# Optimization experiments

Hardware: AMD Instinct MI355X
Metric: run time of the kernel (lower is better)

The kernel has to match this reference:

```python
import jax, jax.numpy as jnp
import numpy as np

N_NODES = 50000
N_EDGES = 800000
D_IN = 128
D_HID = 128
N_LAYERS = 3
BN_EPS = 1e-5


def setup_inputs() -> dict:
    key = jax.random.key(0)
    ks = jax.random.split(key, 12)
    x = jax.random.normal(ks[0], (N_NODES, D_IN), dtype=jnp.float32)
    edge_index = jax.random.randint(ks[1], (2, N_EDGES), 0, N_NODES, dtype=jnp.int64)
    edge_weight = jax.random.uniform(ks[2], (N_EDGES,), dtype=jnp.float32)
    s1 = 1.0 / np.sqrt(D_IN)
    s2 = 1.0 / np.sqrt(D_HID)
    # stacked per-layer GIN MLP params (layer 0 in_dim == hidden_dim so stacking is valid)
    W1s = jax.random.uniform(ks[3], (N_LAYERS, D_HID, D_HID), jnp.float32, -s1, s1)
    b1s = jax.random.uniform(ks[4], (N_LAYERS, D_HID), jnp.float32, -s1, s1)
    W2s = jax.random.uniform(ks[5], (N_LAYERS, D_HID, D_HID), jnp.float32, -s2, s2)
    b2s = jax.random.uniform(ks[6], (N_LAYERS, D_HID), jnp.float32, -s2, s2)
    eps = jnp.zeros((N_LAYERS,), jnp.float32)  # GINConv eps init 0
    gamma = jnp.ones((D_HID,), jnp.float32)
    beta = jnp.zeros((D_HID,), jnp.float32)
    Wp = jax.random.uniform(ks[7], (D_HID, D_HID), jnp.float32, -s2, s2)
    bp = jax.random.uniform(ks[8], (D_HID,), jnp.float32, -s2, s2)
    prelu_a = jnp.asarray(0.25, jnp.float32)
    return {"x": x, "edge_weight": edge_weight, "W1s": W1s, "b1s": b1s,
            "W2s": W2s, "b2s": b2s, "eps": eps, "gamma": gamma, "beta": beta,
            "Wp": Wp, "bp": bp, "prelu_a": prelu_a, "edge_index": edge_index}


def reference(x, edge_weight, W1s, b1s, W2s, b2s, eps, gamma, beta, Wp, bp, prelu_a, edge_index):
    src, dst = edge_index[0], edge_index[1]
    z = x
    for i in range(N_LAYERS):
        # GINConv: sum-aggregate weighted neighbor messages, then 2-layer MLP
        msg = z[src] * edge_weight[:, None]                       # [E, d]
        agg = jax.ops.segment_sum(msg, dst, num_segments=N_NODES)  # [N, d]
        h = (1.0 + eps[i]) * z + agg
        h = jax.nn.relu(h @ W1s[i] + b1s[i]) @ W2s[i] + b2s[i]
        z = jax.nn.relu(h)  # activation; dropout inactive (eval)
    # BatchNorm1d (training-mode batch statistics, biased variance)
    mean = jnp.mean(z, axis=0)
    var = jnp.var(z, axis=0)
    zn = (z - mean) * jax.lax.rsqrt(var + BN_EPS) * gamma + beta
    # projection head: Linear -> PReLU (dropout inactive)
    p = zn @ Wp + bp
    p = jnp.where(p >= 0, p, prelu_a * p)
    return zn, p
```

## Files before the change

kernel.cpp:

```cpp
#include <hip/hip_runtime.h>
#include <hip/hip_fp16.h>

#define N_NODES 50000
#define N_EDGES 800000
#define D 128
#define ND (N_NODES * D)
#define BN_EPS 1e-5f

#define NB 256
#define NPB 196
#define BCAP 4096

typedef short bf16x8 __attribute__((ext_vector_type(8)));
typedef _Float16 f16x8 __attribute__((ext_vector_type(8)));
typedef float f32x4 __attribute__((ext_vector_type(4)));
typedef unsigned short u16x8 __attribute__((ext_vector_type(8)));

__device__ inline unsigned short f2bf(float f) {
    unsigned int u = __float_as_uint(f);
    u += 0x7FFF + ((u >> 16) & 1);
    return (unsigned short)(u >> 16);
}
__device__ inline float bf2f(unsigned short h) {
    return __uint_as_float(((unsigned int)h) << 16);
}
__device__ inline unsigned short f2h(float f) {
    return __half_as_ushort(__float2half(f));
}
__device__ inline float h2f(unsigned short u) {
    return __half2float(__ushort_as_half(u));
}
__device__ inline f16x8 as_f16x8(u16x8 v) {
    union { u16x8 u; f16x8 f; } x; x.u = v; return x.f;
}

__global__ void convert_x(const float* __restrict__ x, ushort* __restrict__ xh) {
    int i = (blockIdx.x * blockDim.x + threadIdx.x) * 4;
    if (i < ND) {
        float4 v = *(const float4*)(x + i);
        *(ushort4*)(xh + i) = make_ushort4(f2h(v.x), f2h(v.y), f2h(v.z), f2h(v.w));
    }
}

__global__ void pack_w_split(const float* __restrict__ W1s, const float* __restrict__ W2s,
                             const float* __restrict__ Wp, ushort* __restrict__ out) {
    int idx = blockIdx.x * blockDim.x + threadIdx.x;
    if (idx >= 7 * 16384) return;
    int m = idx >> 14;
    int p = idx & 16383;
    int c = p >> 11;
    int kc = (p >> 9) & 3;
    int lane = (p >> 3) & 63;
    int j = p & 7;
    int k = kc * 32 + (lane >> 4) * 8 + j;
    int col = c * 16 + (lane & 15);
    const float* src = (m < 3) ? (W1s + (size_t)m * 16384)
                     : (m < 6) ? (W2s + (size_t)(m - 3) * 16384)
                               : Wp;
    float v = src[k * 128 + col];
    if (m < 3) {
        unsigned short hi = f2h(v);
        float r = (v - h2f(hi)) * 2048.0f;
        out[(size_t)(2 * m) * 16384 + p] = hi;
        out[(size_t)(2 * m + 1) * 16384 + p] = f2h(r);
    } else {
        unsigned short hi = f2bf(v);
        float r = v - bf2f(hi);
        out[(size_t)(2 * m) * 16384 + p] = hi;
        out[(size_t)(2 * m + 1) * 16384 + p] = f2bf(r);
    }
}

__global__ void hist_kernel(const int* __restrict__ dst, int* __restrict__ offs) {
    int e = blockIdx.x * blockDim.x + threadIdx.x;
    if (e < N_EDGES) atomicAdd(&offs[dst[e] + 1], 1);
}

__global__ void scan_kernel(int* __restrict__ offs, int* __restrict__ bcur) {
    __shared__ int wsum[16];
    __shared__ int carry_s;
    int tid = threadIdx.x;
    int lane = tid & 63;
    int wave = tid >> 6;
    if (tid == 0) carry_s = 0;
    __syncthreads();
    for (int base = 1; base <= N_NODES; base += 8192) {
        int i0 = base + tid * 8;
        int v[8];
        #pragma unroll
        for (int k = 0; k < 8; ++k) {
            int idx = i0 + k;
            v[k] = (idx <= N_NODES) ? offs[idx] : 0;
        }
        #pragma unroll
        for (int k = 1; k < 8; ++k) v[k] += v[k - 1];
        int tsum = v[7];
        int x = tsum;
        #pragma unroll
        for (int d = 1; d < 64; d <<= 1) {
            int y = __shfl_up(x, d, 64);
            if (lane >= d) x += y;
        }
        if (lane == 63) wsum[wave] = x;
        __syncthreads();
        if (wave == 0 && lane < 16) {
            int y = wsum[lane];
            #pragma unroll
            for (int d = 1; d < 16; d <<= 1) {
                int t = __shfl_up(y, d, 64);
                if (lane >= d) y += t;
            }
            wsum[lane] = y;
        }
        __syncthreads();
        int waveoff = (wave > 0) ? wsum[wave - 1] : 0;
        int total = wsum[15];
        int add = (x - tsum) + waveoff + carry_s;
        #pragma unroll
        for (int k = 0; k < 8; ++k) {
            int idx = i0 + k;
            if (idx <= N_NODES) offs[idx] = v[k] + add;
        }
        __syncthreads();
        if (tid == 0) carry_s += total;
        __syncthreads();
    }
    if (tid < NB) bcur[tid] = offs[tid * NPB];
}

__global__ __launch_bounds__(256) void bucket_scatter(
    const int* __restrict__ src, const int* __restrict__ dst,
    const float* __restrict__ ew, int* __restrict__ bcur,
    uint2* __restrict__ pay) {
    __shared__ int cnt[NB];
    __shared__ int cur[NB];
    int tid = threadIdx.x;
    for (int i = tid; i < NB; i += 256) cnt[i] = 0;
    __syncthreads();
    int base = blockIdx.x * 2048;
    int s[8], d[8], b[8];
    float w[8];
    #pragma unroll
    for (int k = 0; k < 8; ++k) {
        int e = base + k * 256 + tid;
        bool v = e < N_EDGES;
        d[k] = v ? dst[e] : 0;
        s[k] = v ? src[e] : 0;
        w[k] = v ? ew[e] : 0.f;
        b[k] = d[k] / NPB;
        if (v) atomicAdd(&cnt[b[k]], 1);
    }
    __syncthreads();
    for (int i = tid; i < NB; i += 256) {
        int c = cnt[i];
        cur[i] = (c > 0) ? atomicAdd(&bcur[i], c) : 0;
    }
    __syncthreads();
    #pragma unroll
    for (int k = 0; k < 8; ++k) {
        int e = base + k * 256 + tid;
        if (e < N_EDGES) {
            int bk = b[k];
            int p = atomicAdd(&cur[bk], 1);
            unsigned dloc = (unsigned)(d[k] - bk * NPB);
            pay[p] = make_uint2((unsigned)s[k] | (dloc << 17), __float_as_uint(w[k]));
        }
    }
}

__global__ __launch_bounds__(256) void bucket_sort(const int* __restrict__ offs,
                                                   uint2* __restrict__ pay) {
    __shared__ uint2 lp[BCAP];
    __shared__ int cur[NPB];
    int b = blockIdx.x;
    int tid = threadIdx.x;
    int n0 = b * NPB;
    int n1 = min(n0 + NPB, N_NODES);
    int nn = n1 - n0;
    int r0 = offs[n0];
    int r1 = offs[n1];
    for (int i = tid; i < nn; i += 256) cur[i] = offs[n0 + i] - r0;
    __syncthreads();
    int cnt = r1 - r0;
    for (int i = tid; i < cnt; i += 256) {
        uint2 e = pay[r0 + i];
        int dloc = (int)(e.x >> 17);
        int p = atomicAdd(&cur[dloc], 1);
        if (p < BCAP) lp[p] = make_uint2(e.x & 0x1FFFFu, e.y);
    }
    __syncthreads();
    for (int i = tid; i < cnt; i += 256) {
        if (i < BCAP) pay[r0 + i] = lp[i];
    }
}

__global__ void gather_agg_f16(const ushort* __restrict__ z, const int* __restrict__ offs,
                               const uint2* __restrict__ pay,
                               const float* __restrict__ epsp, int layer,
                               ushort* __restrict__ A) {
    int tid = blockIdx.x * blockDim.x + threadIdx.x;
    int n = tid >> 5;
    if (n >= N_NODES) return;
    int f = (tid & 31) << 2;
    float epsv = 1.0f + epsp[layer];
    int beg = offs[n], end = offs[n + 1];
    ushort4 zi = *(const ushort4*)(z + (size_t)n * D + f);
    float ax = epsv * h2f(zi.x), ay = epsv * h2f(zi.y);
    float az = epsv * h2f(zi.z), aw = epsv * h2f(zi.w);
    int j = beg;
    for (; j + 4 <= end; j += 4) {
        uint2 e0 = pay[j];
        uint2 e1 = pay[j + 1];
        uint2 e2 = pay[j + 2];
        uint2 e3 = pay[j + 3];
        ushort4 v0 = *(const ushort4*)(z + (size_t)e0.x * D + f);
        ushort4 v1 = *(const ushort4*)(z + (size_t)e1.x * D + f);
        ushort4 v2 = *(const ushort4*)(z + (size_t)e2.x * D + f);
        ushort4 v3 = *(const ushort4*)(z + (size_t)e3.x * D + f);
        float w0 = __uint_as_float(e0.y);
        float w1 = __uint_as_float(e1.y);
        float w2 = __uint_as_float(e2.y);
        float w3 = __uint_as_float(e3.y);
        ax += h2f(v0.x) * w0 + h2f(v1.x) * w1 + h2f(v2.x) * w2 + h2f(v3.x) * w3;
        ay += h2f(v0.y) * w0 + h2f(v1.y) * w1 + h2f(v2.y) * w2 + h2f(v3.y) * w3;
        az += h2f(v0.z) * w0 + h2f(v1.z) * w1 + h2f(v2.z) * w2 + h2f(v3.z) * w3;
        aw += h2f(v0.w) * w0 + h2f(v1.w) * w1 + h2f(v2.w) * w2 + h2f(v3.w) * w3;
    }
    for (; j < end; ++j) {
        uint2 e0 = pay[j];
        ushort4 v0 = *(const ushort4*)(z + (size_t)e0.x * D + f);
        float w0 = __uint_as_float(e0.y);
        ax += h2f(v0.x) * w0; ay += h2f(v0.y) * w0;
        az += h2f(v0.z) * w0; aw += h2f(v0.w) * w0;
    }
    *(ushort4*)(A + (size_t)n * D + f) = make_ushort4(f2h(ax), f2h(ay), f2h(az), f2h(aw));
}

#define HSTR 132
template<bool STATS>
__global__ __launch_bounds__(256) void mlp_fused(
    const ushort* __restrict__ A,
    const ushort* __restrict__ W1hi, const ushort* __restrict__ W1lo,
    const float* __restrict__ b1,
    const ushort* __restrict__ W2hi, const ushort* __restrict__ W2lo,
    const float* __restrict__ b2, ushort* __restrict__ Z,
    float* __restrict__ stats) {
    __shared__ float Hs[4][16 * HSTR];
    __shared__ float red[256];
    int tid = threadIdx.x;
    int lane = tid & 63;
    int wave = tid >> 6;
    int rlo = lane & 15;
    int quad = lane >> 4;
    int blk0 = blockIdx.x * 64;
    int row0 = blk0 + wave * 16;
    int arow = row0 + rlo;
    int ar = (arow < N_NODES) ? arow : (N_NODES - 1);

    const f16x8* W1h = (const f16x8*)W1hi;
    const f16x8* W1l = (const f16x8*)W1lo;
    const bf16x8* W2h = (const bf16x8*)W2hi;
    const bf16x8* W2l = (const bf16x8*)W2lo;

    f16x8 af[4];
    #pragma unroll
    for (int kc = 0; kc < 4; ++kc) {
        u16x8 raw = *(const u16x8*)(A + (size_t)ar * D + kc * 32 + quad * 8);
        af[kc] = as_f16x8(raw);
    }

    f32x4 acc[8];
    #pragma unroll
    for (int c = 0; c < 8; ++c) {
        f32x4 aH = (f32x4){0.f, 0.f, 0.f, 0.f};
        f32x4 aL = (f32x4){0.f, 0.f, 0.f, 0.f};
        #pragma unroll
        for (int kc = 0; kc < 4; ++kc) {
            f16x8 wh = W1h[(c * 4 + kc) * 64 + lane];
            f16x8 wl = W1l[(c * 4 + kc) * 64 + lane];
            aH = __builtin_amdgcn_mfma_f32_16x16x32_f16(af[kc], wh, aH, 0, 0, 0);
            aL = __builtin_amdgcn_mfma_f32_16x16x32_f16(af[kc], wl, aL, 0, 0, 0);
        }
        acc[c] = aH + aL * (1.0f / 2048.0f);
    }

    #pragma unroll
    for (int c = 0; c < 8; ++c) {
        int col = c * 16 + rlo;
        float bb = b1[col];
        #pragma unroll
        for (int r = 0; r < 4; ++r) {
            Hs[wave][(quad * 4 + r) * HSTR + col] = fmaxf(acc[c][r] + bb, 0.f);
        }
    }
    __syncthreads();

    bf16x8 a2hi[4], a2lo[4];
    #pragma unroll
    for (int kc = 0; kc < 4; ++kc) {
        const float* p = &Hs[wave][rlo * HSTR + kc * 32 + quad * 8];
        #pragma unroll
        for (int j = 0; j < 8; ++j) {
            float v = p[j];
            unsigned short h = f2bf(v);
            a2hi[kc][j] = (short)h;
            a2lo[kc][j] = (short)f2bf(v - bf2f(h));
        }
    }

    f32x4 acc2[8];
    #pragma unroll
    for (int c = 0; c < 8; ++c) acc2[c] = (f32x4){0.f, 0.f, 0.f, 0.f};
    #pragma unroll
    for (int c = 0; c < 8; ++c) {
        #pragma unroll
        for (int kc = 0; kc < 4; ++kc) {
            bf16x8 wh = W2h[(c * 4 + kc) * 64 + lane];
            bf16x8 wl = W2l[(c * 4 + kc) * 64 + lane];
            acc2[c] = __builtin_amdgcn_mfma_f32_16x16x32_bf16(a2lo[kc], wh, acc2[c], 0, 0, 0);
            acc2[c] = __builtin_amdgcn_mfma_f32_16x16x32_bf16(a2hi[kc], wl, acc2[c], 0, 0, 0);
            acc2[c] = __builtin_amdgcn_mfma_f32_16x16x32_bf16(a2hi[kc], wh, acc2[c], 0, 0, 0);
        }
    }

    __syncthreads();
    #pragma unroll
    for (int c = 0; c < 8; ++c) {
        int col = c * 16 + rlo;
        float bb = b2[col];
        #pragma unroll
        for (int r = 0; r < 4; ++r) {
            Hs[wave][(quad * 4 + r) * HSTR + col] = fmaxf(acc2[c][r] + bb, 0.f);
        }
    }
    __syncthreads();
    #pragma unroll
    for (int p2 = 0; p2 < 4; ++p2) {
        int r = p2 * 4 + quad;
        int grow = row0 + r;
        if (grow < N_NODES) {
            float4 lo = *(const float4*)&Hs[wave][r * HSTR + rlo * 8];
            float4 hi = *(const float4*)&Hs[wave][r * HSTR + rlo * 8 + 4];
            ushort us[8] = {f2h(lo.x), f2h(lo.y), f2h(lo.z), f2h(lo.w),
                            f2h(hi.x), f2h(hi.y), f2h(hi.z), f2h(hi.w)};
            *(float4*)(Z + (size_t)grow * D + rlo * 8) = *(const float4*)us;
        }
    }

    if (STATS) {
        int col = tid & 127;
        int half = tid >> 7;
        float s = 0.f, s2 = 0.f;
        #pragma unroll
        for (int i = 0; i < 32; ++i) {
            int row = half * 32 + i;
            if (blk0 + row < N_NODES) {
                float v = Hs[row >> 4][(row & 15) * HSTR + col];
                s += v;
                s2 += v * v;
            }
        }
        red[tid] = s;
        __syncthreads();
        if (half == 0) atomicAdd(&stats[col], s + red[tid + 128]);
        __syncthreads();
        red[tid] = s2;
        __syncthreads();
        if (half == 0) atomicAdd(&stats[D + col], s2 + red[tid + 128]);
    }
}

#define PSTR 132
__global__ __launch_bounds__(256) void bn_proj(
    const ushort* __restrict__ Z, const float* __restrict__ stats,
    const float* __restrict__ gamma, const float* __restrict__ beta,
    const ushort* __restrict__ Wphi, const ushort* __restrict__ Wplo,
    const float* __restrict__ bp, const float* __restrict__ prelu_a,
    float* __restrict__ zn_out, float* __restrict__ p_out) {
    __shared__ float sc_s[D];
    __shared__ float sh_s[D];
    __shared__ float Ps[4][16 * PSTR];
    int tid = threadIdx.x;
    int lane = tid & 63;
    int wave = tid >> 6;
    int rlo = lane & 15;
    int quad = lane >> 4;

    if (tid < D) {
        float m = stats[tid] * (1.0f / N_NODES);
        float v = stats[D + tid] * (1.0f / N_NODES) - m * m;
        float rs = rsqrtf(v + BN_EPS);
        float sc = rs * gamma[tid];
        sc_s[tid] = sc;
        sh_s[tid] = beta[tid] - m * sc;
    }
    __syncthreads();

    int row0 = blockIdx.x * 64 + wave * 16;
    int arow = row0 + rlo;
    int ar = (arow < N_NODES) ? arow : (N_NODES - 1);

    const bf16x8* Wh = (const bf16x8*)Wphi;
    const bf16x8* Wl = (const bf16x8*)Wplo;

    bf16x8 ahi[4], alo[4];
    #pragma unroll
    for (int kc = 0; kc < 4; ++kc) {
        u16x8 raw = *(const u16x8*)(Z + (size_t)ar * D + kc * 32 + quad * 8);
        float zn[8];
        #pragma unroll
        for (int j = 0; j < 8; ++j) {
            int k = kc * 32 + quad * 8 + j;
            zn[j] = sc_s[k] * h2f(raw[j]) + sh_s[k];
            unsigned short h = f2bf(zn[j]);
            ahi[kc][j] = (short)h;
            alo[kc][j] = (short)f2bf(zn[j] - bf2f(h));
        }
        if (arow < N_NODES) {
            float* dst = zn_out + (size_t)arow * D + kc * 32 + quad * 8;
            *(float4*)dst = make_float4(zn[0], zn[1], zn[2], zn[3]);
            *(float4*)(dst + 4) = make_float4(zn[4], zn[5], zn[6], zn[7]);
        }
    }

    f32x4 acc[8];
    #pragma unroll
    for (int c = 0; c < 8; ++c) acc[c] = (f32x4){0.f, 0.f, 0.f, 0.f};
    #pragma unroll
    for (int c = 0; c < 8; ++c) {
        #pragma unroll
        for (int kc = 0; kc < 4; ++kc) {
            bf16x8 wh = Wh[(c * 4 + kc) * 64 + lane];
            bf16x8 wl = Wl[(c * 4 + kc) * 64 + lane];
            acc[c] = __builtin_amdgcn_mfma_f32_16x16x32_bf16(alo[kc], wh, acc[c], 0, 0, 0);
            acc[c] = __builtin_amdgcn_mfma_f32_16x16x32_bf16(ahi[kc], wl, acc[c], 0, 0, 0);
            acc[c] = __builtin_amdgcn_mfma_f32_16x16x32_bf16(ahi[kc], wh, acc[c], 0, 0, 0);
        }
    }

    float aP = prelu_a[0];
    #pragma unroll
    for (int c = 0; c < 8; ++c) {
        int col = c * 16 + rlo;
        float bb = bp[col];
        #pragma unroll
        for (int r = 0; r < 4; ++r) {
            float v = acc[c][r] + bb;
            v = (v >= 0.f) ? v : aP * v;
            Ps[wave][(quad * 4 + r) * PSTR + col] = v;
        }
    }
    __syncthreads();
    #pragma unroll
    for (int p2 = 0; p2 < 8; ++p2) {
        int r = p2 * 2 + (lane >> 5);
        int grow = row0 + r;
        if (grow < N_NODES) {
            *(float4*)(p_out + (size_t)grow * D + (lane & 31) * 4) =
                *(const float4*)&Ps[wave][r * PSTR + (lane & 31) * 4];
        }
    }
}

extern "C" void kernel_launch(void* const* d_in, const int* in_sizes, int n_in,
                              void* d_out, int out_size, void* d_ws, size_t ws_size,
                              hipStream_t stream) {
    (void)in_sizes; (void)n_in; (void)out_size; (void)ws_size;
    const float* x     = (const float*)d_in[0];
    const float* ew    = (const float*)d_in[1];
    const float* W1s   = (const float*)d_in[2];
    const float* b1s   = (const float*)d_in[3];
    const float* W2s   = (const float*)d_in[4];
    const float* b2s   = (const float*)d_in[5];
    const float* eps   = (const float*)d_in[6];
    const float* gamma = (const float*)d_in[7];
    const float* beta  = (const float*)d_in[8];
    const float* Wp    = (const float*)d_in[9];
    const float* bp    = (const float*)d_in[10];
    const float* pa    = (const float*)d_in[11];
    const int*   ei    = (const int*)d_in[12];
    const int* srcp = ei;
    const int* dstp = ei + N_EDGES;

    char* wsb = (char*)d_ws;
    float*  stats  = (float*)wsb;                 wsb += 1024;
    int*    offs   = (int*)wsb;                   wsb += 200016;
    int*    bcur   = (int*)wsb;                   wsb += 200016;
    uint2*  pay    = (uint2*)wsb;                 wsb += 6400000;
    ushort* Wpk    = (ushort*)wsb;                wsb += 14 * 16384 * 2;
    ushort* Xh     = (ushort*)wsb;                wsb += (size_t)ND * 2;
    ushort* Ah     = (ushort*)wsb;                wsb += (size_t)ND * 2;
    ushort* Zh     = (ushort*)wsb;                wsb += (size_t)ND * 2;

    float* out_zn = (float*)d_out;
    float* out_p  = out_zn + ND;

    hipMemsetAsync(stats, 0, 256 * sizeof(float), stream);
    hipMemsetAsync(offs, 0, (N_NODES + 1) * sizeof(int), stream);

    convert_x<<<(ND / 4 + 255) / 256, 256, 0, stream>>>(x, Xh);
    pack_w_split<<<(7 * 16384 + 255) / 256, 256, 0, stream>>>(W1s, W2s, Wp, Wpk);

    hist_kernel<<<(N_EDGES + 255) / 256, 256, 0, stream>>>(dstp, offs);
    scan_kernel<<<1, 1024, 0, stream>>>(offs, bcur);
    bucket_scatter<<<(N_EDGES + 2047) / 2048, 256, 0, stream>>>(srcp, dstp, ew, bcur, pay);
    bucket_sort<<<NB, 256, 0, stream>>>(offs, pay);

    int mgrid = (N_NODES + 63) / 64;
    const ushort* zin = Xh;
    for (int l = 0; l < 3; ++l) {
        gather_agg_f16<<<(N_NODES * 32 + 255) / 256, 256, 0, stream>>>(zin, offs, pay, eps, l, Ah);
        if (l < 2) {
            mlp_fused<false><<<mgrid, 256, 0, stream>>>(Ah,
                Wpk + (size_t)(2 * l) * 16384,       Wpk + (size_t)(2 * l + 1) * 16384, b1s + (size_t)l * D,
                Wpk + (size_t)(2 * (3 + l)) * 16384, Wpk + (size_t)(2 * (3 + l) + 1) * 16384, b2s + (size_t)l * D,
                Zh, stats);
        } else {
            mlp_fused<true><<<mgrid, 256, 0, stream>>>(Ah,
                Wpk + (size_t)(2 * l) * 16384,       Wpk + (size_t)(2 * l + 1) * 16384, b1s + (size_t)l * D,
                Wpk + (size_t)(2 * (3 + l)) * 16384, Wpk + (size_t)(2 * (3 + l) + 1) * 16384, b2s + (size_t)l * D,
                Zh, stats);
        }
        zin = Zh;
    }
    bn_proj<<<mgrid, 256, 0, stream>>>(Zh, stats, gamma, beta,
        Wpk + (size_t)12 * 16384, Wpk + (size_t)13 * 16384, bp, pa, out_zn, out_p);
}
```

Baseline: 413.2 us.

## Restructure GIN MLP kernel to one wave per block with two row tiles

The fused MLP kernel now uses 64-thread blocks, and each wave processes 32 rows as two 16-row MFMA fragments. Each weight fragment loaded from global memory is therefore reused across twice as many rows. The batch-norm statistics are now reduced with cross-lane shuffles inside the output loop instead of a shared-memory reduction over 256 threads, so the block-level barriers go away. In exchange, register pressure per wave goes up and the grid has twice as many small blocks, which shifts occupancy and the rate of atomic updates to the statistics buffer.

```diff
diff --git a/kernel.cpp b/kernel.cpp
--- a/kernel.cpp
+++ b/kernel.cpp
@@ -238,135 +238,134 @@
 
 #define HSTR 132
 template<bool STATS>
-__global__ __launch_bounds__(256) void mlp_fused(
+__global__ __launch_bounds__(64) void mlp_fused(
     const ushort* __restrict__ A,
     const ushort* __restrict__ W1hi, const ushort* __restrict__ W1lo,
     const float* __restrict__ b1,
     const ushort* __restrict__ W2hi, const ushort* __restrict__ W2lo,
     const float* __restrict__ b2, ushort* __restrict__ Z,
     float* __restrict__ stats) {
-    __shared__ float Hs[4][16 * HSTR];
-    __shared__ float red[256];
-    int tid = threadIdx.x;
-    int lane = tid & 63;
-    int wave = tid >> 6;
+    __shared__ float Hs[32 * HSTR];
+    int lane = threadIdx.x;
     int rlo = lane & 15;
     int quad = lane >> 4;
-    int blk0 = blockIdx.x * 64;
-    int row0 = blk0 + wave * 16;
-    int arow = row0 + rlo;
-    int ar = (arow < N_NODES) ? arow : (N_NODES - 1);
+    int row0 = blockIdx.x * 32;
 
     const f16x8* W1h = (const f16x8*)W1hi;
     const f16x8* W1l = (const f16x8*)W1lo;
     const bf16x8* W2h = (const bf16x8*)W2hi;
     const bf16x8* W2l = (const bf16x8*)W2lo;
 
-    f16x8 af[4];
-    #pragma unroll
-    for (int kc = 0; kc < 4; ++kc) {
-        u16x8 raw = *(const u16x8*)(A + (size_t)ar * D + kc * 32 + quad * 8);
-        af[kc] = as_f16x8(raw);
-    }
-
-    f32x4 acc[8];
+    f16x8 af[2][4];
+    #pragma unroll
+    for (int rf = 0; rf < 2; ++rf) {
+        int arow = row0 + rf * 16 + rlo;
+        int ar = (arow < N_NODES) ? arow : (N_NODES - 1);
+        #pragma unroll
+        for (int kc = 0; kc < 4; ++kc) {
+            u16x8 raw = *(const u16x8*)(A + (size_t)ar * D + kc * 32 + quad * 8);
+            af[rf][kc] = as_f16x8(raw);
+        }
+    }
+
     #pragma unroll
     for (int c = 0; c < 8; ++c) {
-        f32x4 aH = (f32x4){0.f, 0.f, 0.f, 0.f};
-        f32x4 aL = (f32x4){0.f, 0.f, 0.f, 0.f};
+        f32x4 aH0 = (f32x4){0.f, 0.f, 0.f, 0.f};
+        f32x4 aL0 = (f32x4){0.f, 0.f, 0.f, 0.f};
+        f32x4 aH1 = (f32x4){0.f, 0.f, 0.f, 0.f};
+        f32x4 aL1 = (f32x4){0.f, 0.f, 0.f, 0.f};
         #pragma unroll
         for (int kc = 0; kc < 4; ++kc) {
             f16x8 wh = W1h[(c * 4 + kc) * 64 + lane];
             f16x8 wl = W1l[(c * 4 + kc) * 64 + lane];
-            aH = __builtin_amdgcn_mfma_f32_16x16x32_f16(af[kc], wh, aH, 0, 0, 0);
-            aL = __builtin_amdgcn_mfma_f32_16x16x32_f16(af[kc], wl, aL, 0, 0, 0);
-        }
-        acc[c] = aH + aL * (1.0f / 2048.0f);
-    }
-
-    #pragma unroll
-    for (int c = 0; c < 8; ++c) {
+            aH0 = __builtin_amdgcn_mfma_f32_16x16x32_f16(af[0][kc], wh, aH0, 0, 0, 0);
+            aH1 = __builtin_amdgcn_mfma_f32_16x16x32_f16(af[1][kc], wh, aH1, 0, 0, 0);
+            aL0 = __builtin_amdgcn_mfma_f32_16x16x32_f16(af[0][kc], wl, aL0, 0, 0, 0);
+            aL1 = __builtin_amdgcn_mfma_f32_16x16x32_f16(af[1][kc], wl, aL1, 0, 0, 0);
+        }
         int col = c * 16 + rlo;
         float bb = b1[col];
         #pragma unroll
         for (int r = 0; r < 4; ++r) {
-            Hs[wave][(quad * 4 + r) * HSTR + col] = fmaxf(acc[c][r] + bb, 0.f);
-        }
-    }
-    __syncthreads();
-
-    bf16x8 a2hi[4], a2lo[4];
-    #pragma unroll
-    for (int kc = 0; kc < 4; ++kc) {
-        const float* p = &Hs[wave][rlo * HSTR + kc * 32 + quad * 8];
-        #pragma unroll
-        for (int j = 0; j < 8; ++j) {
-            float v = p[j];
-            unsigned short h = f2bf(v);
-            a2hi[kc][j] = (short)h;
-            a2lo[kc][j] = (short)f2bf(v - bf2f(h));
-        }
-    }
-
-    f32x4 acc2[8];
-    #pragma unroll
-    for (int c = 0; c < 8; ++c) acc2[c] = (f32x4){0.f, 0.f, 0.f, 0.f};
+            Hs[(quad * 4 + r) * HSTR + col]        = fmaxf(aH0[r] + aL0[r] * (1.0f / 2048.0f) + bb, 0.f);
+            Hs[(16 + quad * 4 + r) * HSTR + col]   = fmaxf(aH1[r] + aL1[r] * (1.0f / 2048.0f) + bb, 0.f);
+        }
+    }
+    __syncthreads();
+
+    bf16x8 a2hi[2][4], a2lo[2][4];
+    #pragma unroll
+    for (int rf = 0; rf < 2; ++rf) {
+        #pragma unroll
+        for (int kc = 0; kc < 4; ++kc) {
+            const float* p = &Hs[(rf * 16 + rlo) * HSTR + kc * 32 + quad * 8];
+            #pragma unroll
+            for (int j = 0; j < 8; ++j) {
+                float v = p[j];
+                unsigned short h = f2bf(v);
+                a2hi[rf][kc][j] = (short)h;
+                a2lo[rf][kc][j] = (short)f2bf(v - bf2f(h));
+            }
+        }
+    }
+    __syncthreads();
+
     #pragma unroll
     for (int c = 0; c < 8; ++c) {
+        f32x4 ac0 = (f32x4){0.f, 0.f, 0.f, 0.f};
+        f32x4 ac1 = (f32x4){0.f, 0.f, 0.f, 0.f};
         #pragma unroll
         for (int kc = 0; kc < 4; ++kc) {
             bf16x8 wh = W2h[(c * 4 + kc) * 64 + lane];
             bf16x8 wl = W2l[(c * 4 + kc) * 64 + lane];
-            acc2[c] = __builtin_amdgcn_mfma_f32_16x16x32_bf16(a2lo[kc], wh, acc2[c], 0, 0, 0);
-            acc2[c] = __builtin_amdgcn_mfma_f32_16x16x32_bf16(a2hi[kc], wl, acc2[c], 0, 0, 0);
-            acc2[c] = __builtin_amdgcn_mfma_f32_16x16x32_bf16(a2hi[kc], wh, acc2[c], 0, 0, 0);
-        }
-    }
-
-    __syncthreads();
-    #pragma unroll
-    for (int c = 0; c < 8; ++c) {
+            ac0 = __builtin_amdgcn_mfma_f32_16x16x32_bf16(a2lo[0][kc], wh, ac0, 0, 0, 0);
+            ac1 = __builtin_amdgcn_mfma_f32_16x16x32_bf16(a2lo[1][kc], wh, ac1, 0, 0, 0);
+            ac0 = __builtin_amdgcn_mfma_f32_16x16x32_bf16(a2hi[0][kc], wl, ac0, 0, 0, 0);
+            ac1 = __builtin_amdgcn_mfma_f32_16x16x32_bf16(a2hi[1][kc], wl, ac1, 0, 0, 0);
+            ac0 = __builtin_amdgcn_mfma_f32_16x16x32_bf16(a2hi[0][kc], wh, ac0, 0, 0, 0);
+            ac1 = __builtin_amdgcn_mfma_f32_16x16x32_bf16(a2hi[1][kc], wh, ac1, 0, 0, 0);
+        }
         int col = c * 16 + rlo;
         float bb = b2[col];
+        float s = 0.f, s2 = 0.f;
         #pragma unroll
         for (int r = 0; r < 4; ++r) {
-            Hs[wave][(quad * 4 + r) * HSTR + col] = fmaxf(acc2[c][r] + bb, 0.f);
-        }
-    }
-    __syncthreads();
-    #pragma unroll
-    for (int p2 = 0; p2 < 4; ++p2) {
-        int r = p2 * 4 + quad;
+            float v0 = fmaxf(ac0[r] + bb, 0.f);
+            float v1 = fmaxf(ac1[r] + bb, 0.f);
+            Hs[(quad * 4 + r) * HSTR + col] = v0;
+            Hs[(16 + quad * 4 + r) * HSTR + col] = v1;
+            if (STATS) {
+                float m0 = (row0 + quad * 4 + r < N_NODES) ? v0 : 0.f;
+                float m1 = (row0 + 16 + quad * 4 + r < N_NODES) ? v1 : 0.f;
+                s += m0 + m1;
+                s2 += m0 * m0 + m1 * m1;
+            }
+        }
+        if (STATS) {
+            s  += __shfl_xor(s, 16, 64);
+            s  += __shfl_xor(s, 32, 64);
+            s2 += __shfl_xor(s2, 16, 64);
+            s2 += __shfl_xor(s2, 32, 64);
+            if (lane < 16) {
+                atomicAdd(&stats[col], s);
+                atomicAdd(&stats[D + col], s2);
+            }
+        }
+    }
+    __syncthreads();
+
+    #pragma unroll
+    for (int it = 0; it < 8; ++it) {
+        int r = it * 4 + quad;
         int grow = row0 + r;
         if (grow < N_NODES) {
-            float4 lo = *(const float4*)&Hs[wave][r * HSTR + rlo * 8];
-            float4 hi = *(const float4*)&Hs[wave][r * HSTR + rlo * 8 + 4];
+            const float* p = &Hs[r * HSTR + rlo * 8];
+            float4 lo = *(const float4*)p;
+            float4 hi = *(const float4*)(p + 4);
             ushort us[8] = {f2h(lo.x), f2h(lo.y), f2h(lo.z), f2h(lo.w),
                             f2h(hi.x), f2h(hi.y), f2h(hi.z), f2h(hi.w)};
             *(float4*)(Z + (size_t)grow * D + rlo * 8) = *(const float4*)us;
         }
-    }
-
-    if (STATS) {
-        int col = tid & 127;
-        int half = tid >> 7;
-        float s = 0.f, s2 = 0.f;
-        #pragma unroll
-        for (int i = 0; i < 32; ++i) {
-            int row = half * 32 + i;
-            if (blk0 + row < N_NODES) {
-                float v = Hs[row >> 4][(row & 15) * HSTR + col];
-                s += v;
-                s2 += v * v;
-            }
-        }
-        red[tid] = s;
-        __syncthreads();
-        if (half == 0) atomicAdd(&stats[col], s + red[tid + 128]);
-        __syncthreads();
-        red[tid] = s2;
-        __syncthreads();
-        if (half == 0) atomicAdd(&stats[D + col], s2 + red[tid + 128]);
     }
 }
 
@@ -506,23 +505,24 @@
     bucket_scatter<<<(N_EDGES + 2047) / 2048, 256, 0, stream>>>(srcp, dstp, ew, bcur, pay);
     bucket_sort<<<NB, 256, 0, stream>>>(offs, pay);
 
-    int mgrid = (N_NODES + 63) / 64;
+    int mgrid = (N_NODES + 31) / 32;
+    int pgrid = (N_NODES + 63) / 64;
     const ushort* zin = Xh;
     for (int l = 0; l < 3; ++l) {
         gather_agg_f16<<<(N_NODES * 32 + 255) / 256, 256, 0, stream>>>(zin, offs, pay, eps, l, Ah);
         if (l < 2) {
-            mlp_fused<false><<<mgrid, 256, 0, stream>>>(Ah,
+            mlp_fused<false><<<mgrid, 64, 0, stream>>>(Ah,
                 Wpk + (size_t)(2 * l) * 16384,       Wpk + (size_t)(2 * l + 1) * 16384, b1s + (size_t)l * D,
                 Wpk + (size_t)(2 * (3 + l)) * 16384, Wpk + (size_t)(2 * (3 + l) + 1) * 16384, b2s + (size_t)l * D,
                 Zh, stats);
         } else {
-            mlp_fused<true><<<mgrid, 256, 0, stream>>>(Ah,
+            mlp_fused<true><<<mgrid, 64, 0, stream>>>(Ah,
                 Wpk + (size_t)(2 * l) * 16384,       Wpk + (size_t)(2 * l + 1) * 16384, b1s + (size_t)l * D,
                 Wpk + (size_t)(2 * (3 + l)) * 16384, Wpk + (size_t)(2 * (3 + l) + 1) * 16384, b2s + (size_t)l * D,
                 Zh, stats);
         }
         zin = Zh;
     }
-    bn_proj<<<mgrid, 256, 0, stream>>>(Zh, stats, gamma, beta,
+    bn_proj<<<pgrid, 256, 0, stream>>>(Zh, stats, gamma, beta,
         Wpk + (size_t)12 * 16384, Wpk + (size_t)13 * 16384, bp, pa, out_zn, out_p);
 }
```

Measured after the change: 437.0 us. 1.06x slower.

## Split MLP columns across waves so each weight fragment serves four row tiles

Applied to the files above, without the earlier changes.

Each wave in the fused GIN MLP kernel used to own 16 rows and loaded every weight fragment for all 128 output columns. Now each wave owns 32 output columns for all 64 rows of the block, so each weight fragment is loaded once and used in four MFMAs. The hidden activations are shared through one block-wide LDS tile, and the BatchNorm statistics are reduced inside the epilogue with cross-lane shuffles instead of a separate LDS reduction pass. In exchange, each wave now loads A fragments for all 64 rows and keeps more accumulators live, which raises register pressure.

```diff
diff --git a/kernel.cpp b/kernel.cpp
--- a/kernel.cpp
+++ b/kernel.cpp
@@ -245,128 +245,143 @@
     const ushort* __restrict__ W2hi, const ushort* __restrict__ W2lo,
     const float* __restrict__ b2, ushort* __restrict__ Z,
     float* __restrict__ stats) {
-    __shared__ float Hs[4][16 * HSTR];
-    __shared__ float red[256];
+    __shared__ float Hs[64 * HSTR];
     int tid = threadIdx.x;
     int lane = tid & 63;
     int wave = tid >> 6;
     int rlo = lane & 15;
     int quad = lane >> 4;
     int blk0 = blockIdx.x * 64;
-    int row0 = blk0 + wave * 16;
-    int arow = row0 + rlo;
-    int ar = (arow < N_NODES) ? arow : (N_NODES - 1);
 
     const f16x8* W1h = (const f16x8*)W1hi;
     const f16x8* W1l = (const f16x8*)W1lo;
     const bf16x8* W2h = (const bf16x8*)W2hi;
     const bf16x8* W2l = (const bf16x8*)W2lo;
 
-    f16x8 af[4];
-    #pragma unroll
-    for (int kc = 0; kc < 4; ++kc) {
-        u16x8 raw = *(const u16x8*)(A + (size_t)ar * D + kc * 32 + quad * 8);
-        af[kc] = as_f16x8(raw);
-    }
-
-    f32x4 acc[8];
-    #pragma unroll
-    for (int c = 0; c < 8; ++c) {
-        f32x4 aH = (f32x4){0.f, 0.f, 0.f, 0.f};
-        f32x4 aL = (f32x4){0.f, 0.f, 0.f, 0.f};
+    f16x8 af[4][4];
+    #pragma unroll
+    for (int rf = 0; rf < 4; ++rf) {
+        int arow = blk0 + rf * 16 + rlo;
+        int ar = (arow < N_NODES) ? arow : (N_NODES - 1);
+        #pragma unroll
+        for (int kc = 0; kc < 4; ++kc) {
+            u16x8 raw = *(const u16x8*)(A + (size_t)ar * D + kc * 32 + quad * 8);
+            af[rf][kc] = as_f16x8(raw);
+        }
+    }
+
+    #pragma unroll
+    for (int cc = 0; cc < 2; ++cc) {
+        int c = 2 * wave + cc;
+        f32x4 aH[4], aL[4];
+        #pragma unroll
+        for (int rf = 0; rf < 4; ++rf) {
+            aH[rf] = (f32x4){0.f, 0.f, 0.f, 0.f};
+            aL[rf] = (f32x4){0.f, 0.f, 0.f, 0.f};
+        }
         #pragma unroll
         for (int kc = 0; kc < 4; ++kc) {
             f16x8 wh = W1h[(c * 4 + kc) * 64 + lane];
             f16x8 wl = W1l[(c * 4 + kc) * 64 + lane];
-            aH = __builtin_amdgcn_mfma_f32_16x16x32_f16(af[kc], wh, aH, 0, 0, 0);
-            aL = __builtin_amdgcn_mfma_f32_16x16x32_f16(af[kc], wl, aL, 0, 0, 0);
-        }
-        acc[c] = aH + aL * (1.0f / 2048.0f);
-    }
-
-    #pragma unroll
-    for (int c = 0; c < 8; ++c) {
+            #pragma unroll
+            for (int rf = 0; rf < 4; ++rf) {
+                aH[rf] = __builtin_amdgcn_mfma_f32_16x16x32_f16(af[rf][kc], wh, aH[rf], 0, 0, 0);
+                aL[rf] = __builtin_amdgcn_mfma_f32_16x16x32_f16(af[rf][kc], wl, aL[rf], 0, 0, 0);
+            }
+        }
         int col = c * 16 + rlo;
         float bb = b1[col];
         #pragma unroll
-        for (int r = 0; r < 4; ++r) {
-            Hs[wave][(quad * 4 + r) * HSTR + col] = fmaxf(acc[c][r] + bb, 0.f);
-        }
-    }
-    __syncthreads();
-
-    bf16x8 a2hi[4], a2lo[4];
+        for (int rf = 0; rf < 4; ++rf) {
+            #pragma unroll
+            for (int r = 0; r < 4; ++r) {
+                Hs[(rf * 16 + quad * 4 + r) * HSTR + col] =
+                    fmaxf(aH[rf][r] + aL[rf][r] * (1.0f / 2048.0f) + bb, 0.f);
+            }
+        }
+    }
+    __syncthreads();
+
+    f32x4 acc2[2][4];
+    #pragma unroll
+    for (int cc = 0; cc < 2; ++cc)
+        #pragma unroll
+        for (int rf = 0; rf < 4; ++rf)
+            acc2[cc][rf] = (f32x4){0.f, 0.f, 0.f, 0.f};
+
     #pragma unroll
     for (int kc = 0; kc < 4; ++kc) {
-        const float* p = &Hs[wave][rlo * HSTR + kc * 32 + quad * 8];
-        #pragma unroll
-        for (int j = 0; j < 8; ++j) {
-            float v = p[j];
-            unsigned short h = f2bf(v);
-            a2hi[kc][j] = (short)h;
-            a2lo[kc][j] = (short)f2bf(v - bf2f(h));
-        }
-    }
-
-    f32x4 acc2[8];
-    #pragma unroll
-    for (int c = 0; c < 8; ++c) acc2[c] = (f32x4){0.f, 0.f, 0.f, 0.f};
-    #pragma unroll
-    for (int c = 0; c < 8; ++c) {
-        #pragma unroll
-        for (int kc = 0; kc < 4; ++kc) {
+        bf16x8 a2hi[4], a2lo[4];
+        #pragma unroll
+        for (int rf = 0; rf < 4; ++rf) {
+            const float* p = &Hs[(rf * 16 + rlo) * HSTR + kc * 32 + quad * 8];
+            #pragma unroll
+            for (int j = 0; j < 8; ++j) {
+                float v = p[j];
+                unsigned short h = f2bf(v);
+                a2hi[rf][j] = (short)h;
+                a2lo[rf][j] = (short)f2bf(v - bf2f(h));
+            }
+        }
+        #pragma unroll
+        for (int cc = 0; cc < 2; ++cc) {
+            int c = 2 * wave + cc;
             bf16x8 wh = W2h[(c * 4 + kc) * 64 + lane];
             bf16x8 wl = W2l[(c * 4 + kc) * 64 + lane];
-            acc2[c] = __builtin_amdgcn_mfma_f32_16x16x32_bf16(a2lo[kc], wh, acc2[c], 0, 0, 0);
-            acc2[c] = __builtin_amdgcn_mfma_f32_16x16x32_bf16(a2hi[kc], wl, acc2[c], 0, 0, 0);
-            acc2[c] = __builtin_amdgcn_mfma_f32_16x16x32_bf16(a2hi[kc], wh, acc2[c], 0, 0, 0);
-        }
-    }
-
-    __syncthreads();
-    #pragma unroll
-    for (int c = 0; c < 8; ++c) {
+            #pragma unroll
+            for (int rf = 0; rf < 4; ++rf) {
+                acc2[cc][rf] = __builtin_amdgcn_mfma_f32_16x16x32_bf16(a2lo[rf], wh, acc2[cc][rf], 0, 0, 0);
+                acc2[cc][rf] = __builtin_amdgcn_mfma_f32_16x16x32_bf16(a2hi[rf], wl, acc2[cc][rf], 0, 0, 0);
+                acc2[cc][rf] = __builtin_amdgcn_mfma_f32_16x16x32_bf16(a2hi[rf], wh, acc2[cc][rf], 0, 0, 0);
+            }
+        }
+    }
+    __syncthreads();
+
+    #pragma unroll
+    for (int cc = 0; cc < 2; ++cc) {
+        int c = 2 * wave + cc;
         int col = c * 16 + rlo;
         float bb = b2[col];
-        #pragma unroll
-        for (int r = 0; r < 4; ++r) {
-            Hs[wave][(quad * 4 + r) * HSTR + col] = fmaxf(acc2[c][r] + bb, 0.f);
-        }
-    }
-    __syncthreads();
-    #pragma unroll
-    for (int p2 = 0; p2 < 4; ++p2) {
-        int r = p2 * 4 + quad;
-        int grow = row0 + r;
+        float s = 0.f, s2 = 0.f;
+        #pragma unroll
+        for (int rf = 0; rf < 4; ++rf) {
+            #pragma unroll
+            for (int r = 0; r < 4; ++r) {
+                float v = fmaxf(acc2[cc][rf][r] + bb, 0.f);
+                Hs[(rf * 16 + quad * 4 + r) * HSTR + col] = v;
+                if (STATS) {
+                    float m = (blk0 + rf * 16 + quad * 4 + r < N_NODES) ? v : 0.f;
+                    s += m;
+                    s2 += m * m;
+                }
+            }
+        }
+        if (STATS) {
+            s  += __shfl_xor(s, 16, 64);
+            s  += __shfl_xor(s, 32, 64);
+            s2 += __shfl_xor(s2, 16, 64);
+            s2 += __shfl_xor(s2, 32, 64);
+            if (quad == 0) {
+                atomicAdd(&stats[col], s);
+                atomicAdd(&stats[D + col], s2);
+            }
+        }
+    }
+    __syncthreads();
+
+    #pragma unroll
+    for (int it = 0; it < 4; ++it) {
+        int r = wave * 16 + it * 4 + quad;
+        int grow = blk0 + r;
         if (grow < N_NODES) {
-            float4 lo = *(const float4*)&Hs[wave][r * HSTR + rlo * 8];
-            float4 hi = *(const float4*)&Hs[wave][r * HSTR + rlo * 8 + 4];
+            const float* p = &Hs[r * HSTR + rlo * 8];
+            float4 lo = *(const float4*)p;
+            float4 hi = *(const float4*)(p + 4);
             ushort us[8] = {f2h(lo.x), f2h(lo.y), f2h(lo.z), f2h(lo.w),
                             f2h(hi.x), f2h(hi.y), f2h(hi.z), f2h(hi.w)};
             *(float4*)(Z + (size_t)grow * D + rlo * 8) = *(const float4*)us;
         }
-    }
-
-    if (STATS) {
-        int col = tid & 127;
-        int half = tid >> 7;
-        float s = 0.f, s2 = 0.f;
-        #pragma unroll
-        for (int i = 0; i < 32; ++i) {
-            int row = half * 32 + i;
-            if (blk0 + row < N_NODES) {
-                float v = Hs[row >> 4][(row & 15) * HSTR + col];
-                s += v;
-                s2 += v * v;
-            }
-        }
-        red[tid] = s;
-        __syncthreads();
-        if (half == 0) atomicAdd(&stats[col], s + red[tid + 128]);
-        __syncthreads();
-        red[tid] = s2;
-        __syncthreads();
-        if (half == 0) atomicAdd(&stats[D + col], s2 + red[tid + 128]);
     }
 }
 
```

Result: faster. 404.3 us (-2.2%).
